# Kernel optimization log

Hardware: AMD Instinct MI355X
Metric: run time of the kernel (lower is better)

The kernel has to match this reference:

```python
import jax, jax.numpy as jnp
import numpy as np

N = 10000      # nodes
DEG = 32       # avg degree
D_IN = 256     # in_feats
H = 128        # hidden_layers[0] == hidden_layers[2]
K = 3          # hidden_layers[1] = Chebyshev order
D_OUT = 64     # out_feat


def setup_inputs() -> dict:
    key = jax.random.key(0)
    ks = jax.random.split(key, 8)
    x = jax.random.normal(ks[0], (N, D_IN), jnp.float32)
    # sparse binary adjacency built by scattering into a dense [N, N] matrix
    src = jax.random.randint(ks[1], (N * DEG,), 0, N)
    dst = jax.random.randint(ks[2], (N * DEG,), 0, N)
    adj = jnp.zeros((N, N), jnp.float32).at[src, dst].set(1.0)
    init = lambda k, shape, fan: jax.random.normal(k, shape, jnp.float32) / np.sqrt(fan)
    W_in = init(ks[3], (D_IN, H), D_IN)
    b_in = jnp.zeros((H,), jnp.float32)
    W_cheb = init(ks[4], (K * H, H), K * H)   # dgl ChebConv: Linear(k*in, out)
    b_cheb = jnp.zeros((H,), jnp.float32)
    W_out = init(ks[5], (H, D_OUT), H)
    b_out = jnp.zeros((D_OUT,), jnp.float32)
    return dict(x=x, adj=adj, W_in=W_in, b_in=b_in, W_cheb=W_cheb,
                b_cheb=b_cheb, W_out=W_out, b_out=b_out)


def reference(x, adj, W_in, b_in, W_cheb, b_cheb, W_out, b_out):
    n = x.shape[0]
    # graph construction from dense adjacency (eager, like adj.to_dense().nonzero())
    src, dst = jnp.nonzero(adj)
    # symmetric normalization on in-degrees (dgl ChebConv, norm clamped at 1)
    deg = jax.ops.segment_sum(jnp.ones(src.shape[0], jnp.float32), dst, num_segments=n)
    norm = jnp.clip(deg, 1.0) ** -0.5  # [n]
    re_norm = 2.0 / 2.0  # lambda_max = [2] -> re_norm = 1

    def prop(h):
        # D^{-1/2} A D^{-1/2} h : gather at src, scatter-add at dst
        return jax.ops.segment_sum((h * norm[:, None])[src], dst, num_segments=n) * norm[:, None]

    # input linear + relu
    h = jax.nn.relu(x @ W_in + b_in)
    # Chebyshev recursion (dgl ChebConv with lambda_max=2)
    X0 = h
    X1 = -re_norm * prop(X0) + (re_norm - 1.0) * X0
    Xs = [X0, X1]
    Xpp, Xp = X0, X1
    for _ in range(2, K):
        Xi = -2.0 * re_norm * prop(Xp) + 2.0 * (re_norm - 1.0) * Xp - Xpp
        Xs.append(Xi)
        Xpp, Xp = Xp, Xi
    hc = jax.nn.relu(jnp.concatenate(Xs, axis=1) @ W_cheb + b_cheb)  # [n, H]
    return hc @ W_out + b_out  # [n, D_OUT]
```

## Files before the change

### kernel.cpp

```cpp
#include <hip/hip_runtime.h>
#include <hip/hip_bf16.h>
#include <cstdint>
#include <cstddef>

#define NN 10000
#define MAXDEG 128
#define LDX 384

#define GEMM_BLKS 313
#define CONV_BLK  1
#define SCAN_BLKS 3072
#define FAT_BLKS  (GEMM_BLKS + CONV_BLK + SCAN_BLKS)

typedef __attribute__((ext_vector_type(8))) short bf16x8;
typedef __attribute__((ext_vector_type(4))) float f32x4;

__device__ __forceinline__ float bf2f(unsigned short u) {
    union { unsigned int i; float f; } c; c.i = ((unsigned int)u) << 16; return c.f;
}
__device__ __forceinline__ unsigned short f2bf(float f) {
    union { float f; unsigned int i; } c; c.f = f;
    unsigned int x = c.i;
    return (unsigned short)((x + 0x7fffu + ((x >> 16) & 1u)) >> 16);
}

__global__ __launch_bounds__(256) void fat_scan_gemm(
        const float4* __restrict__ adj4, int total4,
        int* __restrict__ cnt, int* __restrict__ csr,
        const float* __restrict__ x, const float* __restrict__ W_in,
        const float* __restrict__ b_in,
        const float* __restrict__ W_cheb, const float* __restrict__ W_out,
        unsigned short* __restrict__ Xc,
        unsigned short* __restrict__ Wtc, unsigned short* __restrict__ Wto) {
    __shared__ float smem[10240];
    int bid = blockIdx.x;
    int t = threadIdx.x;

    if (bid < GEMM_BLKS) {
        constexpr int K = 256, N = 128, BM = 32, KC = 64;
        float* Wl = smem;
        float* Al = smem + KC * N;
        int r0 = bid * BM;
        int c2 = t & 63;
        int g  = t >> 6;
        float2 acc[8];
        #pragma unroll
        for (int i = 0; i < 8; ++i) acc[i] = make_float2(0.f, 0.f);

        for (int kk = 0; kk < K; kk += KC) {
            __syncthreads();
            #pragma unroll
            for (int i = 0; i < KC * N / 4 / 256; ++i) {
                int idx = t + i * 256;
                ((float4*)Wl)[idx] = ((const float4*)(W_in + (size_t)kk * N))[idx];
            }
            #pragma unroll
            for (int i = 0; i < BM * KC / 4 / 256; ++i) {
                int idx = t + i * 256;
                int row = idx >> 4;
                int cf  = idx & 15;
                float4 v = make_float4(0.f, 0.f, 0.f, 0.f);
                if (r0 + row < NN)
                    v = *(const float4*)(x + (size_t)(r0 + row) * K + kk + cf * 4);
                *(float4*)(Al + row * KC + cf * 4) = v;
            }
            __syncthreads();
            for (int k = 0; k < KC; k += 4) {
                float4 av[8];
                #pragma unroll
                for (int rr = 0; rr < 8; ++rr)
                    av[rr] = *(const float4*)(Al + (g * 8 + rr) * KC + k);
                #pragma unroll
                for (int k2 = 0; k2 < 4; ++k2) {
                    float2 wv = *(const float2*)(Wl + (k + k2) * N + c2 * 2);
                    #pragma unroll
                    for (int rr = 0; rr < 8; ++rr) {
                        float a = (k2 == 0) ? av[rr].x : (k2 == 1) ? av[rr].y
                                  : (k2 == 2) ? av[rr].z : av[rr].w;
                        acc[rr].x = fmaf(a, wv.x, acc[rr].x);
                        acc[rr].y = fmaf(a, wv.y, acc[rr].y);
                    }
                }
            }
        }
        float2 bv = *(const float2*)(b_in + c2 * 2);
        #pragma unroll
        for (int rr = 0; rr < 8; ++rr) {
            int r = r0 + g * 8 + rr;
            if (r < NN) {
                float vx = fmaxf(acc[rr].x + bv.x, 0.f);
                float vy = fmaxf(acc[rr].y + bv.y, 0.f);
                uint32_t o = (uint32_t)f2bf(vx) | ((uint32_t)f2bf(vy) << 16);
                *(uint32_t*)(Xc + (size_t)r * LDX + c2 * 2) = o;
            }
        }
    } else if (bid == GEMM_BLKS) {
        for (int idx = t; idx < 384 * 128; idx += 256) {
            int k = idx >> 7, c = idx & 127;
            Wtc[c * 384 + k] = f2bf(W_cheb[idx]);
        }
        for (int idx = t; idx < 128 * 64; idx += 256) {
            int k = idx >> 6, c = idx & 63;
            Wto[c * 128 + k] = f2bf(W_out[idx]);
        }
    } else {
        int sid = bid - (GEMM_BLKS + CONV_BLK);
        int idx = sid * 256 + t;
        int stride = SCAN_BLKS * 256;
        for (int p = idx; p < total4; p += stride) {
            float4 v = adj4[p];
            if (v.x != 0.f || v.y != 0.f || v.z != 0.f || v.w != 0.f) {
                int lin = p * 4;
                #pragma unroll
                for (int c = 0; c < 4; ++c) {
                    float f = (c == 0) ? v.x : (c == 1) ? v.y : (c == 2) ? v.z : v.w;
                    if (f != 0.f) {
                        int l = lin + c;
                        int i = l / NN;
                        int j = l - i * NN;
                        int pos = atomicAdd(&cnt[j], 1);
                        if (pos < MAXDEG) csr[j * MAXDEG + pos] = i;
                    }
                }
            }
        }
    }
}

template<bool SUB>
__global__ __launch_bounds__(256) void prop_k(unsigned short* __restrict__ X,
                                              const int* __restrict__ csr,
                                              const int* __restrict__ cnt,
                                              int srcOff, int dstOff, float scale) {
    int j = blockIdx.x * 4 + (threadIdx.x >> 6);
    if (j >= NN) return;
    int lane = threadIdx.x & 63;
    int cj = cnt[j];
    int cn = min(cj, MAXDEG);
    const int* nb = csr + j * MAXDEG;
    float ax0 = 0.f, ay0 = 0.f, ax1 = 0.f, ay1 = 0.f;
    int e = 0;
    for (; e + 2 <= cn; e += 2) {
        int i0 = nb[e], i1 = nb[e + 1];
        int c0 = cnt[i0], c1 = cnt[i1];
        uint32_t h0 = *(const uint32_t*)(X + (size_t)i0 * LDX + srcOff + lane * 2);
        uint32_t h1 = *(const uint32_t*)(X + (size_t)i1 * LDX + srcOff + lane * 2);
        float w0 = rsqrtf(fmaxf((float)c0, 1.f));
        float w1 = rsqrtf(fmaxf((float)c1, 1.f));
        ax0 = fmaf(w0, bf2f((unsigned short)h0), ax0);
        ay0 = fmaf(w0, bf2f((unsigned short)(h0 >> 16)), ay0);
        ax1 = fmaf(w1, bf2f((unsigned short)h1), ax1);
        ay1 = fmaf(w1, bf2f((unsigned short)(h1 >> 16)), ay1);
    }
    if (e < cn) {
        int i0 = nb[e];
        float w0 = rsqrtf(fmaxf((float)cnt[i0], 1.f));
        uint32_t h0 = *(const uint32_t*)(X + (size_t)i0 * LDX + srcOff + lane * 2);
        ax0 = fmaf(w0, bf2f((unsigned short)h0), ax0);
        ay0 = fmaf(w0, bf2f((unsigned short)(h0 >> 16)), ay0);
    }
    float s = scale * rsqrtf(fmaxf((float)cj, 1.f));
    float rx = s * (ax0 + ax1), ry = s * (ay0 + ay1);
    if (SUB) {
        uint32_t x0 = *(const uint32_t*)(X + (size_t)j * LDX + lane * 2);
        rx -= bf2f((unsigned short)x0);
        ry -= bf2f((unsigned short)(x0 >> 16));
    }
    uint32_t o = (uint32_t)f2bf(rx) | ((uint32_t)f2bf(ry) << 16);
    *(uint32_t*)(X + (size_t)j * LDX + dstOff + lane * 2) = o;
}

__global__ __launch_bounds__(256) void cheb_out_mfma(
        const unsigned short* __restrict__ Xc,
        const unsigned short* __restrict__ Wtc,
        const float* __restrict__ bc,
        const unsigned short* __restrict__ Wto,
        const float* __restrict__ bo,
        float* __restrict__ out) {
    __shared__ unsigned short hcL[32][136];
    int t = threadIdx.x;
    int w = t >> 6, lane = t & 63;
    int r0 = blockIdx.x * 32;
    int lr = lane & 15;
    int kg = lane >> 4;

    f32x4 acc[2][2] = {};
    for (int k0 = 0; k0 < 384; k0 += 32) {
        bf16x8 a[2], b[2];
        #pragma unroll
        for (int m = 0; m < 2; ++m) {
            int row = r0 + m * 16 + lr;
            row = min(row, NN - 1);
            a[m] = *(const bf16x8*)(Xc + (size_t)row * LDX + k0 + kg * 8);
        }
        #pragma unroll
        for (int n = 0; n < 2; ++n) {
            int col = w * 32 + n * 16 + lr;
            b[n] = *(const bf16x8*)(Wtc + (size_t)col * 384 + k0 + kg * 8);
        }
        #pragma unroll
        for (int m = 0; m < 2; ++m)
            #pragma unroll
            for (int n = 0; n < 2; ++n)
                acc[m][n] = __builtin_amdgcn_mfma_f32_16x16x32_bf16(a[m], b[n], acc[m][n], 0, 0, 0);
    }
    #pragma unroll
    for (int m = 0; m < 2; ++m) {
        #pragma unroll
        for (int n = 0; n < 2; ++n) {
            int col = w * 32 + n * 16 + lr;
            float bv = bc[col];
            #pragma unroll
            for (int r = 0; r < 4; ++r) {
                int row = m * 16 + kg * 4 + r;
                hcL[row][col] = f2bf(fmaxf(acc[m][n][r] + bv, 0.f));
            }
        }
    }
    __syncthreads();
    int rt = w >> 1, ch = w & 1;
    f32x4 a2[2] = {};
    for (int k0 = 0; k0 < 128; k0 += 32) {
        bf16x8 af = *(const bf16x8*)(&hcL[rt * 16 + lr][k0 + kg * 8]);
        #pragma unroll
        for (int n = 0; n < 2; ++n) {
            int col = ch * 32 + n * 16 + lr;
            bf16x8 bf_ = *(const bf16x8*)(Wto + (size_t)col * 128 + k0 + kg * 8);
            a2[n] = __builtin_amdgcn_mfma_f32_16x16x32_bf16(af, bf_, a2[n], 0, 0, 0);
        }
    }
    #pragma unroll
    for (int n = 0; n < 2; ++n) {
        int col = ch * 32 + n * 16 + lr;
        float bv = bo[col];
        #pragma unroll
        for (int r = 0; r < 4; ++r) {
            int row = r0 + rt * 16 + kg * 4 + r;
            if (row < NN) out[(size_t)row * 64 + col] = a2[n][r] + bv;
        }
    }
}

extern "C" void kernel_launch(void* const* d_in, const int* in_sizes, int n_in,
                              void* d_out, int out_size, void* d_ws, size_t ws_size,
                              hipStream_t stream) {
    const float* x      = (const float*)d_in[0];
    const float* adj    = (const float*)d_in[1];
    const float* W_in   = (const float*)d_in[2];
    const float* b_in   = (const float*)d_in[3];
    const float* W_cheb = (const float*)d_in[4];
    const float* b_cheb = (const float*)d_in[5];
    const float* W_out  = (const float*)d_in[6];
    const float* b_out  = (const float*)d_in[7];
    float* out = (float*)d_out;

    char* ws = (char*)d_ws;
    int*            cnt = (int*)(ws + 0);
    int*            csr = (int*)(ws + 40960);
    unsigned short* Xc  = (unsigned short*)(ws + 5160960);
    unsigned short* Wtc = (unsigned short*)(ws + 12845056);
    unsigned short* Wto = (unsigned short*)(ws + 12943360);

    int adj_total = in_sizes[1];

    hipMemsetAsync(cnt, 0, NN * sizeof(int), stream);
    fat_scan_gemm<<<FAT_BLKS, 256, 0, stream>>>(
        (const float4*)adj, adj_total / 4, cnt, csr,
        x, W_in, b_in, W_cheb, W_out, Xc, Wtc, Wto);
    prop_k<false><<<(NN + 3) / 4, 256, 0, stream>>>(Xc, csr, cnt, 0, 128, -1.0f);
    prop_k<true><<<(NN + 3) / 4, 256, 0, stream>>>(Xc, csr, cnt, 128, 256, -2.0f);
    cheb_out_mfma<<<(NN + 31) / 32, 256, 0, stream>>>(Xc, Wtc, b_cheb, Wto, b_out, out);
}
```

Baseline: 238.5 us.

## Compact adjacency scan into wave-buffered edge list, build CSR in separate pass

The dense adjacency scan now collects nonzeros into per-wave LDS buffers and flushes them in batches to a global packed edge list with one atomic per flush. A new csr_build kernel turns that list into the per-destination CSR using scattered atomics. The aim is to keep the 400MB streaming scan free of scattered global atomics and writes, and the scan also prefetches the next float4. It also halves the GEMM K-chunk (which shrinks shared memory for occupancy), cuts the scan block count, and swaps the memset for a zero kernel. The cost is an extra kernel launch and an extra pass over the edge list.

```diff
diff --git a/kernel.cpp b/kernel.cpp
--- a/kernel.cpp
+++ b/kernel.cpp
@@ -8,9 +8,9 @@
 #define LDX 384
 
 #define GEMM_BLKS 313
-#define CONV_BLK  1
-#define SCAN_BLKS 3072
-#define FAT_BLKS  (GEMM_BLKS + CONV_BLK + SCAN_BLKS)
+#define SCAN_BLKS 2048
+#define FAT_BLKS  (GEMM_BLKS + 1 + SCAN_BLKS)
+#define FLUSH_THRESH 256
 
 typedef __attribute__((ext_vector_type(8))) short bf16x8;
 typedef __attribute__((ext_vector_type(4))) float f32x4;
@@ -24,20 +24,26 @@
     return (unsigned short)((x + 0x7fffu + ((x >> 16) & 1u)) >> 16);
 }
 
+__global__ __launch_bounds__(256) void zero_k(int* __restrict__ cnt, int* __restrict__ eCnt) {
+    int i = blockIdx.x * 256 + threadIdx.x;
+    if (i < NN) cnt[i] = 0;
+    if (i == 0) *eCnt = 0;
+}
+
 __global__ __launch_bounds__(256) void fat_scan_gemm(
         const float4* __restrict__ adj4, int total4,
-        int* __restrict__ cnt, int* __restrict__ csr,
+        unsigned int* __restrict__ edges, int* __restrict__ eCnt,
         const float* __restrict__ x, const float* __restrict__ W_in,
         const float* __restrict__ b_in,
         const float* __restrict__ W_cheb, const float* __restrict__ W_out,
         unsigned short* __restrict__ Xc,
         unsigned short* __restrict__ Wtc, unsigned short* __restrict__ Wto) {
-    __shared__ float smem[10240];
+    __shared__ float smem[5120];
     int bid = blockIdx.x;
     int t = threadIdx.x;
 
     if (bid < GEMM_BLKS) {
-        constexpr int K = 256, N = 128, BM = 32, KC = 64;
+        constexpr int K = 256, N = 128, BM = 32, KC = 32;
         float* Wl = smem;
         float* Al = smem + KC * N;
         int r0 = bid * BM;
@@ -54,11 +60,9 @@
                 int idx = t + i * 256;
                 ((float4*)Wl)[idx] = ((const float4*)(W_in + (size_t)kk * N))[idx];
             }
-            #pragma unroll
-            for (int i = 0; i < BM * KC / 4 / 256; ++i) {
-                int idx = t + i * 256;
-                int row = idx >> 4;
-                int cf  = idx & 15;
+            {
+                int row = t >> 3;
+                int cf  = t & 7;
                 float4 v = make_float4(0.f, 0.f, 0.f, 0.f);
                 if (r0 + row < NN)
                     v = *(const float4*)(x + (size_t)(r0 + row) * K + kk + cf * 4);
@@ -104,26 +108,73 @@
             Wto[c * 128 + k] = f2bf(W_out[idx]);
         }
     } else {
-        int sid = bid - (GEMM_BLKS + CONV_BLK);
-        int idx = sid * 256 + t;
+        int* wcntL = (int*)smem;
+        unsigned int* wbufL = (unsigned int*)(smem + 64);
+        int w = t >> 6, lane = t & 63;
+        if (lane == 0) wcntL[w] = 0;
+        int sid = bid - (GEMM_BLKS + 1);
         int stride = SCAN_BLKS * 256;
-        for (int p = idx; p < total4; p += stride) {
-            float4 v = adj4[p];
-            if (v.x != 0.f || v.y != 0.f || v.z != 0.f || v.w != 0.f) {
-                int lin = p * 4;
-                #pragma unroll
-                for (int c = 0; c < 4; ++c) {
-                    float f = (c == 0) ? v.x : (c == 1) ? v.y : (c == 2) ? v.z : v.w;
-                    if (f != 0.f) {
-                        int l = lin + c;
-                        int i = l / NN;
-                        int j = l - i * NN;
-                        int pos = atomicAdd(&cnt[j], 1);
-                        if (pos < MAXDEG) csr[j * MAXDEG + pos] = i;
+        int p0 = sid * 256 + t;
+        int iters = (total4 + stride - 1) / stride;
+
+        float4 v = (p0 < total4) ? adj4[p0] : make_float4(0.f, 0.f, 0.f, 0.f);
+        for (int it = 1; it <= iters; ++it) {
+            int pn = p0 + it * stride;
+            float4 vn = (it < iters && pn < total4) ? adj4[pn]
+                        : make_float4(0.f, 0.f, 0.f, 0.f);
+            int p = p0 + (it - 1) * stride;
+            unsigned m = (v.x != 0.f ? 1u : 0u) | (v.y != 0.f ? 2u : 0u)
+                       | (v.z != 0.f ? 4u : 0u) | (v.w != 0.f ? 8u : 0u);
+            if (__any((int)m)) {
+                if (m) {
+                    int n = __popc(m);
+                    int base = atomicAdd(&wcntL[w], n);
+                    int lin = p * 4;
+                    #pragma unroll
+                    for (int c = 0; c < 4; ++c) {
+                        if ((m >> c) & 1u) {
+                            int l = lin + c;
+                            int i = l / NN;
+                            int j = l - i * NN;
+                            wbufL[w * 512 + base++] = (unsigned)((j << 14) | i);
+                        }
                     }
                 }
-            }
-        }
+                int n = wcntL[w];
+                if (n >= FLUSH_THRESH) {
+                    int gb = 0;
+                    if (lane == 0) gb = atomicAdd(eCnt, n);
+                    gb = __shfl(gb, 0);
+                    for (int e = lane; e < n; e += 64)
+                        edges[gb + e] = wbufL[w * 512 + e];
+                    if (lane == 0) wcntL[w] = 0;
+                }
+            }
+            v = vn;
+        }
+        int n = wcntL[w];
+        if (n) {
+            int gb = 0;
+            if (lane == 0) gb = atomicAdd(eCnt, n);
+            gb = __shfl(gb, 0);
+            for (int e = lane; e < n; e += 64)
+                edges[gb + e] = wbufL[w * 512 + e];
+        }
+    }
+}
+
+__global__ __launch_bounds__(256) void csr_build(const unsigned int* __restrict__ edges,
+                                                 const int* __restrict__ eCnt,
+                                                 int* __restrict__ cnt,
+                                                 int* __restrict__ csr) {
+    int E = *eCnt;
+    int stride = gridDim.x * 256;
+    for (int e = blockIdx.x * 256 + threadIdx.x; e < E; e += stride) {
+        unsigned u = edges[e];
+        int i = (int)(u & 16383u);
+        int j = (int)(u >> 14);
+        int pos = atomicAdd(&cnt[j], 1);
+        if (pos < MAXDEG) csr[j * MAXDEG + pos] = i;
     }
 }
 
@@ -255,18 +306,21 @@
     float* out = (float*)d_out;
 
     char* ws = (char*)d_ws;
-    int*            cnt = (int*)(ws + 0);
-    int*            csr = (int*)(ws + 40960);
-    unsigned short* Xc  = (unsigned short*)(ws + 5160960);
-    unsigned short* Wtc = (unsigned short*)(ws + 12845056);
-    unsigned short* Wto = (unsigned short*)(ws + 12943360);
+    int*            cnt   = (int*)(ws + 0);
+    int*            eCnt  = (int*)(ws + 40960);
+    int*            csr   = (int*)(ws + 45056);
+    unsigned int*   edges = (unsigned int*)(ws + 5165056);
+    unsigned short* Xc    = (unsigned short*)(ws + 6765568);
+    unsigned short* Wtc   = (unsigned short*)(ws + 14445568);
+    unsigned short* Wto   = (unsigned short*)(ws + 14543872);
 
     int adj_total = in_sizes[1];
 
-    hipMemsetAsync(cnt, 0, NN * sizeof(int), stream);
+    zero_k<<<(NN + 255) / 256, 256, 0, stream>>>(cnt, eCnt);
     fat_scan_gemm<<<FAT_BLKS, 256, 0, stream>>>(
-        (const float4*)adj, adj_total / 4, cnt, csr,
+        (const float4*)adj, adj_total / 4, edges, eCnt,
         x, W_in, b_in, W_cheb, W_out, Xc, Wtc, Wto);
+    csr_build<<<512, 256, 0, stream>>>(edges, eCnt, cnt, csr);
     prop_k<false><<<(NN + 3) / 4, 256, 0, stream>>>(Xc, csr, cnt, 0, 128, -1.0f);
     prop_k<true><<<(NN + 3) / 4, 256, 0, stream>>>(Xc, csr, cnt, 128, 256, -2.0f);
     cheb_out_mfma<<<(NN + 31) / 32, 256, 0, stream>>>(Xc, Wtc, b_cheb, Wto, b_out, out);
```

Result: slower. 277.7 us (+16.5%).

## Compact adjacency scan per wave, build CSR in separate kernel with prefetching

Applied to the files above, without the earlier changes.

The dense adjacency scan now records nonzero edges into per-wave segments using ballot/popcount compaction, with a software-prefetched double-buffered load loop, instead of issuing a global atomic per edge during the scan. A new csr_build kernel then performs the atomics to fill the CSR. The cnt reset moves from a memset into the conversion block, and the GEMM K-chunk is halved to cut shared memory for higher occupancy. The aim is to keep the 400MB scan purely bandwidth-bound. The cost is an extra launch and an edge buffer. There is also a race risk: cnt is zeroed inside the same kernel, though only csr_build reads it afterwards.

```diff
diff --git a/kernel.cpp b/kernel.cpp
--- a/kernel.cpp
+++ b/kernel.cpp
@@ -8,9 +8,10 @@
 #define LDX 384
 
 #define GEMM_BLKS 313
-#define CONV_BLK  1
-#define SCAN_BLKS 3072
-#define FAT_BLKS  (GEMM_BLKS + CONV_BLK + SCAN_BLKS)
+#define SCAN_BLKS 2048
+#define FAT_BLKS  (GEMM_BLKS + 1 + SCAN_BLKS)
+#define SEG 256
+#define NWAVES (SCAN_BLKS * 4)
 
 typedef __attribute__((ext_vector_type(8))) short bf16x8;
 typedef __attribute__((ext_vector_type(4))) float f32x4;
@@ -24,20 +25,43 @@
     return (unsigned short)((x + 0x7fffu + ((x >> 16) & 1u)) >> 16);
 }
 
+__device__ __forceinline__ void scan_compact(float4 v, int p, int lane,
+                                             unsigned int* __restrict__ myseg,
+                                             int& base) {
+    unsigned m = (v.x != 0.f ? 1u : 0u) | (v.y != 0.f ? 2u : 0u)
+               | (v.z != 0.f ? 4u : 0u) | (v.w != 0.f ? 8u : 0u);
+    #pragma unroll
+    for (int c = 0; c < 4; ++c) {
+        unsigned long long bal = __ballot((m >> c) & 1u);
+        if (bal) {
+            if ((m >> c) & 1u) {
+                int off = (int)__popcll(bal & ((1ull << lane) - 1ull));
+                int l = p * 4 + c;
+                int i = l / NN;
+                int j = l - i * NN;
+                if (base + off < SEG)
+                    myseg[base + off] = (unsigned)((j << 14) | i);
+            }
+            base += (int)__popcll(bal);
+        }
+    }
+}
+
 __global__ __launch_bounds__(256) void fat_scan_gemm(
         const float4* __restrict__ adj4, int total4,
-        int* __restrict__ cnt, int* __restrict__ csr,
+        unsigned int* __restrict__ edges, int* __restrict__ waveCnt,
+        int* __restrict__ cnt,
         const float* __restrict__ x, const float* __restrict__ W_in,
         const float* __restrict__ b_in,
         const float* __restrict__ W_cheb, const float* __restrict__ W_out,
         unsigned short* __restrict__ Xc,
         unsigned short* __restrict__ Wtc, unsigned short* __restrict__ Wto) {
-    __shared__ float smem[10240];
+    __shared__ float smem[5120];
     int bid = blockIdx.x;
     int t = threadIdx.x;
 
     if (bid < GEMM_BLKS) {
-        constexpr int K = 256, N = 128, BM = 32, KC = 64;
+        constexpr int K = 256, N = 128, BM = 32, KC = 32;
         float* Wl = smem;
         float* Al = smem + KC * N;
         int r0 = bid * BM;
@@ -54,11 +78,9 @@
                 int idx = t + i * 256;
                 ((float4*)Wl)[idx] = ((const float4*)(W_in + (size_t)kk * N))[idx];
             }
-            #pragma unroll
-            for (int i = 0; i < BM * KC / 4 / 256; ++i) {
-                int idx = t + i * 256;
-                int row = idx >> 4;
-                int cf  = idx & 15;
+            {
+                int row = t >> 3;
+                int cf  = t & 7;
                 float4 v = make_float4(0.f, 0.f, 0.f, 0.f);
                 if (r0 + row < NN)
                     v = *(const float4*)(x + (size_t)(r0 + row) * K + kk + cf * 4);
@@ -103,27 +125,54 @@
             int k = idx >> 6, c = idx & 63;
             Wto[c * 128 + k] = f2bf(W_out[idx]);
         }
+        for (int idx = t; idx < NN; idx += 256) cnt[idx] = 0;
     } else {
-        int sid = bid - (GEMM_BLKS + CONV_BLK);
-        int idx = sid * 256 + t;
+        int sid = bid - (GEMM_BLKS + 1);
+        int w = t >> 6, lane = t & 63;
+        int wid = sid * 4 + w;
+        unsigned int* myseg = edges + (size_t)wid * SEG;
+        int base = 0;
+
         int stride = SCAN_BLKS * 256;
-        for (int p = idx; p < total4; p += stride) {
-            float4 v = adj4[p];
-            if (v.x != 0.f || v.y != 0.f || v.z != 0.f || v.w != 0.f) {
-                int lin = p * 4;
-                #pragma unroll
-                for (int c = 0; c < 4; ++c) {
-                    float f = (c == 0) ? v.x : (c == 1) ? v.y : (c == 2) ? v.z : v.w;
-                    if (f != 0.f) {
-                        int l = lin + c;
-                        int i = l / NN;
-                        int j = l - i * NN;
-                        int pos = atomicAdd(&cnt[j], 1);
-                        if (pos < MAXDEG) csr[j * MAXDEG + pos] = i;
-                    }
-                }
-            }
-        }
+        int p0 = sid * 256 + t;
+        const float4 Z = make_float4(0.f, 0.f, 0.f, 0.f);
+        int iters = (total4 + 2 * stride - 1) / (2 * stride);
+
+        int pa = p0, pb = p0 + stride;
+        float4 va = (pa < total4) ? adj4[pa] : Z;
+        float4 vb = (pb < total4) ? adj4[pb] : Z;
+        int pc = p0 + 2 * stride, pd = p0 + 3 * stride;
+        float4 vc = (pc < total4) ? adj4[pc] : Z;
+        float4 vd = (pd < total4) ? adj4[pd] : Z;
+
+        for (int it = 0; it < iters; ++it) {
+            int pe = p0 + (2 * it + 4) * stride;
+            int pf = p0 + (2 * it + 5) * stride;
+            float4 ve = (it + 2 < iters && pe < total4) ? adj4[pe] : Z;
+            float4 vf = (it + 2 < iters && pf < total4) ? adj4[pf] : Z;
+            int p = p0 + (2 * it) * stride;
+            scan_compact(va, p, lane, myseg, base);
+            scan_compact(vb, p + stride, lane, myseg, base);
+            va = vc; vb = vd; vc = ve; vd = vf;
+        }
+        if (lane == 0) waveCnt[wid] = (base < SEG) ? base : SEG;
+    }
+}
+
+__global__ __launch_bounds__(256) void csr_build(const unsigned int* __restrict__ edges,
+                                                 const int* __restrict__ waveCnt,
+                                                 int* __restrict__ cnt,
+                                                 int* __restrict__ csr) {
+    int wid = blockIdx.x * 4 + (threadIdx.x >> 6);
+    int lane = threadIdx.x & 63;
+    int n = waveCnt[wid];
+    const unsigned int* seg = edges + (size_t)wid * SEG;
+    for (int e = lane; e < n; e += 64) {
+        unsigned u = seg[e];
+        int i = (int)(u & 16383u);
+        int j = (int)(u >> 14);
+        int pos = atomicAdd(&cnt[j], 1);
+        if (pos < MAXDEG) csr[j * MAXDEG + pos] = i;
     }
 }
 
@@ -255,18 +304,20 @@
     float* out = (float*)d_out;
 
     char* ws = (char*)d_ws;
-    int*            cnt = (int*)(ws + 0);
-    int*            csr = (int*)(ws + 40960);
-    unsigned short* Xc  = (unsigned short*)(ws + 5160960);
-    unsigned short* Wtc = (unsigned short*)(ws + 12845056);
-    unsigned short* Wto = (unsigned short*)(ws + 12943360);
+    int*            cnt     = (int*)(ws + 0);
+    int*            waveCnt = (int*)(ws + 40960);
+    int*            csr     = (int*)(ws + 73728);
+    unsigned int*   edges   = (unsigned int*)(ws + 5193728);
+    unsigned short* Xc      = (unsigned short*)(ws + 13582336);
+    unsigned short* Wtc     = (unsigned short*)(ws + 21262336);
+    unsigned short* Wto     = (unsigned short*)(ws + 21360640);
 
     int adj_total = in_sizes[1];
 
-    hipMemsetAsync(cnt, 0, NN * sizeof(int), stream);
     fat_scan_gemm<<<FAT_BLKS, 256, 0, stream>>>(
-        (const float4*)adj, adj_total / 4, cnt, csr,
+        (const float4*)adj, adj_total / 4, edges, waveCnt, cnt,
         x, W_in, b_in, W_cheb, W_out, Xc, Wtc, Wto);
+    csr_build<<<SCAN_BLKS, 256, 0, stream>>>(edges, waveCnt, cnt, csr);
     prop_k<false><<<(NN + 3) / 4, 256, 0, stream>>>(Xc, csr, cnt, 0, 128, -1.0f);
     prop_k<true><<<(NN + 3) / 4, 256, 0, stream>>>(Xc, csr, cnt, 128, 256, -2.0f);
     cheb_out_mfma<<<(NN + 31) / 32, 256, 0, stream>>>(Xc, Wtc, b_cheb, Wto, b_out, out);
```

After: 224.4 us. 5.9% less time.

## Split adjacency scan into bitmap detect pass and decode pass fused with GEMM

Applied to the files above, without the earlier changes.

The dense adjacency scan now runs in two stages. A streaming pass with deep register prefetch packs nonzero flags into a bitmap, and a second kernel decodes that bitmap into the CSR with atomics while the input GEMM runs in other blocks. The count zeroing moves from a memset into the first kernel, and the propagation loop is unrolled to four neighbors. The aim is to make the 400MB adjacency read purely bandwidth-bound, without atomic or divergent work in the streaming loop. It adds a bitmap workspace and an extra launch, and comparing raw bits instead of floats treats -0.0 as a nonzero entry.

```diff
diff --git a/kernel.cpp b/kernel.cpp
--- a/kernel.cpp
+++ b/kernel.cpp
@@ -7,10 +7,14 @@
 #define MAXDEG 128
 #define LDX 384
 
+#define PA_BLKS 2048
+#define PA_STEPS 48
+#define PA_REG (PA_STEPS * 256)
+#define ZERO_BLKS 40
+#define PA_GRID (PA_BLKS + ZERO_BLKS + 1)
+
 #define GEMM_BLKS 313
-#define CONV_BLK  1
-#define SCAN_BLKS 3072
-#define FAT_BLKS  (GEMM_BLKS + CONV_BLK + SCAN_BLKS)
+#define PB_GRID (GEMM_BLKS + PA_BLKS)
 
 typedef __attribute__((ext_vector_type(8))) short bf16x8;
 typedef __attribute__((ext_vector_type(4))) float f32x4;
@@ -24,23 +28,72 @@
     return (unsigned short)((x + 0x7fffu + ((x >> 16) & 1u)) >> 16);
 }
 
-__global__ __launch_bounds__(256) void fat_scan_gemm(
-        const float4* __restrict__ adj4, int total4,
+__global__ __launch_bounds__(256) void scan_detect(
+        const uint4* __restrict__ adj4, int total4,
+        unsigned int* __restrict__ bm, int* __restrict__ cnt,
+        const float* __restrict__ W_cheb, const float* __restrict__ W_out,
+        unsigned short* __restrict__ Wtc, unsigned short* __restrict__ Wto) {
+    int b = blockIdx.x;
+    int t = threadIdx.x;
+
+    if (b >= PA_BLKS) {
+        int xb = b - PA_BLKS;
+        if (xb < ZERO_BLKS) {
+            int i = xb * 256 + t;
+            if (i < NN) cnt[i] = 0;
+        } else {
+            for (int idx = t; idx < 384 * 128; idx += 256) {
+                int k = idx >> 7, c = idx & 127;
+                Wtc[c * 384 + k] = f2bf(W_cheb[idx]);
+            }
+            for (int idx = t; idx < 128 * 64; idx += 256) {
+                int k = idx >> 6, c = idx & 63;
+                Wto[c * 128 + k] = f2bf(W_out[idx]);
+            }
+        }
+        return;
+    }
+
+    int p0 = b * PA_REG + t;
+    int LIM = total4 - 1;
+
+    uint4 buf[4];
+    #pragma unroll
+    for (int d = 0; d < 4; ++d)
+        buf[d] = adj4[min(p0 + d * 256, LIM)];
+
+    unsigned acc[6] = {0u, 0u, 0u, 0u, 0u, 0u};
+
+    #pragma unroll
+    for (int s = 0; s < PA_STEPS; ++s) {
+        uint4 u = buf[s & 3];
+        buf[s & 3] = adj4[min(p0 + (s + 4) * 256, LIM)];
+        int p = p0 + s * 256;
+        unsigned nib = (u.x != 0u ? 1u : 0u) | (u.y != 0u ? 2u : 0u)
+                     | (u.z != 0u ? 4u : 0u) | (u.w != 0u ? 8u : 0u);
+        if (p > LIM) nib = 0u;
+        acc[s >> 3] |= nib << ((s & 7) * 4);
+    }
+
+    #pragma unroll
+    for (int r = 0; r < 6; ++r)
+        bm[(b * 6 + r) * 256 + t] = acc[r];
+}
+
+__global__ __launch_bounds__(256) void decode_gemm(
+        const unsigned int* __restrict__ bm,
         int* __restrict__ cnt, int* __restrict__ csr,
         const float* __restrict__ x, const float* __restrict__ W_in,
-        const float* __restrict__ b_in,
-        const float* __restrict__ W_cheb, const float* __restrict__ W_out,
-        unsigned short* __restrict__ Xc,
-        unsigned short* __restrict__ Wtc, unsigned short* __restrict__ Wto) {
-    __shared__ float smem[10240];
-    int bid = blockIdx.x;
+        const float* __restrict__ b_in, unsigned short* __restrict__ Xc) {
+    __shared__ float smem[5120];
+    int b = blockIdx.x;
     int t = threadIdx.x;
 
-    if (bid < GEMM_BLKS) {
-        constexpr int K = 256, N = 128, BM = 32, KC = 64;
+    if (b < GEMM_BLKS) {
+        constexpr int K = 256, N = 128, BM = 32, KC = 32;
         float* Wl = smem;
         float* Al = smem + KC * N;
-        int r0 = bid * BM;
+        int r0 = b * BM;
         int c2 = t & 63;
         int g  = t >> 6;
         float2 acc[8];
@@ -54,11 +107,9 @@
                 int idx = t + i * 256;
                 ((float4*)Wl)[idx] = ((const float4*)(W_in + (size_t)kk * N))[idx];
             }
-            #pragma unroll
-            for (int i = 0; i < BM * KC / 4 / 256; ++i) {
-                int idx = t + i * 256;
-                int row = idx >> 4;
-                int cf  = idx & 15;
+            {
+                int row = t >> 3;
+                int cf  = t & 7;
                 float4 v = make_float4(0.f, 0.f, 0.f, 0.f);
                 if (r0 + row < NN)
                     v = *(const float4*)(x + (size_t)(r0 + row) * K + kk + cf * 4);
@@ -94,34 +145,22 @@
                 *(uint32_t*)(Xc + (size_t)r * LDX + c2 * 2) = o;
             }
         }
-    } else if (bid == GEMM_BLKS) {
-        for (int idx = t; idx < 384 * 128; idx += 256) {
-            int k = idx >> 7, c = idx & 127;
-            Wtc[c * 384 + k] = f2bf(W_cheb[idx]);
-        }
-        for (int idx = t; idx < 128 * 64; idx += 256) {
-            int k = idx >> 6, c = idx & 63;
-            Wto[c * 128 + k] = f2bf(W_out[idx]);
-        }
     } else {
-        int sid = bid - (GEMM_BLKS + CONV_BLK);
-        int idx = sid * 256 + t;
-        int stride = SCAN_BLKS * 256;
-        for (int p = idx; p < total4; p += stride) {
-            float4 v = adj4[p];
-            if (v.x != 0.f || v.y != 0.f || v.z != 0.f || v.w != 0.f) {
-                int lin = p * 4;
-                #pragma unroll
-                for (int c = 0; c < 4; ++c) {
-                    float f = (c == 0) ? v.x : (c == 1) ? v.y : (c == 2) ? v.z : v.w;
-                    if (f != 0.f) {
-                        int l = lin + c;
-                        int i = l / NN;
-                        int j = l - i * NN;
-                        int pos = atomicAdd(&cnt[j], 1);
-                        if (pos < MAXDEG) csr[j * MAXDEG + pos] = i;
-                    }
-                }
+        int sb = b - GEMM_BLKS;
+        #pragma unroll
+        for (int r = 0; r < 6; ++r) {
+            unsigned w = bm[(sb * 6 + r) * 256 + t];
+            while (w) {
+                int bit = __ffs(w) - 1;
+                w &= w - 1u;
+                int s = r * 8 + (bit >> 2);
+                int c = bit & 3;
+                int p = sb * PA_REG + s * 256 + t;
+                int l = p * 4 + c;
+                int i = l / NN;
+                int j = l - i * NN;
+                int pos = atomicAdd(&cnt[j], 1);
+                if (pos < MAXDEG) csr[j * MAXDEG + pos] = i;
             }
         }
     }
@@ -139,20 +178,29 @@
     int cn = min(cj, MAXDEG);
     const int* nb = csr + j * MAXDEG;
     float ax0 = 0.f, ay0 = 0.f, ax1 = 0.f, ay1 = 0.f;
+    float ax2 = 0.f, ay2 = 0.f, ax3 = 0.f, ay3 = 0.f;
     int e = 0;
-    for (; e + 2 <= cn; e += 2) {
-        int i0 = nb[e], i1 = nb[e + 1];
-        int c0 = cnt[i0], c1 = cnt[i1];
+    for (; e + 4 <= cn; e += 4) {
+        int i0 = nb[e], i1 = nb[e + 1], i2 = nb[e + 2], i3 = nb[e + 3];
+        int c0 = cnt[i0], c1 = cnt[i1], c2 = cnt[i2], c3 = cnt[i3];
         uint32_t h0 = *(const uint32_t*)(X + (size_t)i0 * LDX + srcOff + lane * 2);
         uint32_t h1 = *(const uint32_t*)(X + (size_t)i1 * LDX + srcOff + lane * 2);
+        uint32_t h2 = *(const uint32_t*)(X + (size_t)i2 * LDX + srcOff + lane * 2);
+        uint32_t h3 = *(const uint32_t*)(X + (size_t)i3 * LDX + srcOff + lane * 2);
         float w0 = rsqrtf(fmaxf((float)c0, 1.f));
         float w1 = rsqrtf(fmaxf((float)c1, 1.f));
+        float w2 = rsqrtf(fmaxf((float)c2, 1.f));
+        float w3 = rsqrtf(fmaxf((float)c3, 1.f));
         ax0 = fmaf(w0, bf2f((unsigned short)h0), ax0);
         ay0 = fmaf(w0, bf2f((unsigned short)(h0 >> 16)), ay0);
         ax1 = fmaf(w1, bf2f((unsigned short)h1), ax1);
         ay1 = fmaf(w1, bf2f((unsigned short)(h1 >> 16)), ay1);
-    }
-    if (e < cn) {
+        ax2 = fmaf(w2, bf2f((unsigned short)h2), ax2);
+        ay2 = fmaf(w2, bf2f((unsigned short)(h2 >> 16)), ay2);
+        ax3 = fmaf(w3, bf2f((unsigned short)h3), ax3);
+        ay3 = fmaf(w3, bf2f((unsigned short)(h3 >> 16)), ay3);
+    }
+    for (; e < cn; ++e) {
         int i0 = nb[e];
         float w0 = rsqrtf(fmaxf((float)cnt[i0], 1.f));
         uint32_t h0 = *(const uint32_t*)(X + (size_t)i0 * LDX + srcOff + lane * 2);
@@ -160,7 +208,8 @@
         ay0 = fmaf(w0, bf2f((unsigned short)(h0 >> 16)), ay0);
     }
     float s = scale * rsqrtf(fmaxf((float)cj, 1.f));
-    float rx = s * (ax0 + ax1), ry = s * (ay0 + ay1);
+    float rx = s * ((ax0 + ax1) + (ax2 + ax3));
+    float ry = s * ((ay0 + ay1) + (ay2 + ay3));
     if (SUB) {
         uint32_t x0 = *(const uint32_t*)(X + (size_t)j * LDX + lane * 2);
         rx -= bf2f((unsigned short)x0);
@@ -257,16 +306,16 @@
     char* ws = (char*)d_ws;
     int*            cnt = (int*)(ws + 0);
     int*            csr = (int*)(ws + 40960);
-    unsigned short* Xc  = (unsigned short*)(ws + 5160960);
-    unsigned short* Wtc = (unsigned short*)(ws + 12845056);
-    unsigned short* Wto = (unsigned short*)(ws + 12943360);
+    unsigned int*   bm  = (unsigned int*)(ws + 5160960);
+    unsigned short* Xc  = (unsigned short*)(ws + 17743872);
+    unsigned short* Wtc = (unsigned short*)(ws + 25427968);
+    unsigned short* Wto = (unsigned short*)(ws + 25526272);
 
     int adj_total = in_sizes[1];
 
-    hipMemsetAsync(cnt, 0, NN * sizeof(int), stream);
-    fat_scan_gemm<<<FAT_BLKS, 256, 0, stream>>>(
-        (const float4*)adj, adj_total / 4, cnt, csr,
-        x, W_in, b_in, W_cheb, W_out, Xc, Wtc, Wto);
+    scan_detect<<<PA_GRID, 256, 0, stream>>>(
+        (const uint4*)adj, adj_total / 4, bm, cnt, W_cheb, W_out, Wtc, Wto);
+    decode_gemm<<<PB_GRID, 256, 0, stream>>>(bm, cnt, csr, x, W_in, b_in, Xc);
     prop_k<false><<<(NN + 3) / 4, 256, 0, stream>>>(Xc, csr, cnt, 0, 128, -1.0f);
     prop_k<true><<<(NN + 3) / 4, 256, 0, stream>>>(Xc, csr, cnt, 128, 256, -2.0f);
     cheb_out_mfma<<<(NN + 31) / 32, 256, 0, stream>>>(Xc, Wtc, b_cheb, Wto, b_out, out);
```

After: 237.4 us. No clear change (-0.5%).
